# Kernel tuning notes

Measured on AMD Instinct MI355X. Metric: run time of the kernel, lower is better.

## Reference

```python
import jax, jax.numpy as jnp
import numpy as np

B, N, M, H, D = 16, 512, 16, 8, 128  # batch, nodes, neighbors, heads, input_dim
NEG_SLOPE = 0.2
EPS = 1e-5

def _glorot(key, shape):
    fan = sum(shape[-2:]) if len(shape) >= 2 else shape[-1]
    return jax.random.normal(key, shape, dtype=jnp.float32) * (2.0 / fan) ** 0.5

def setup_inputs() -> dict:
    key = jax.random.key(0)
    ks = jax.random.split(key, 12)
    h = jax.random.normal(ks[0], (B, N, D), dtype=jnp.float32)
    adj = jax.random.randint(ks[1], (B, N, M), 0, 2, dtype=jnp.int32)
    n_list = jax.random.randint(ks[2], (B, N, M), 0, N, dtype=jnp.int32)
    W = _glorot(ks[3], (H, D, D))            # per-head projection
    a_src = _glorot(ks[4], (H, D))           # attention vector, source half
    a_dst = _glorot(ks[5], (H, D))           # attention vector, neighbor half
    Wo = _glorot(ks[6], (H * D, D))          # concat-heads output projection
    ln1_g = jnp.ones((D,), jnp.float32); ln1_b = jnp.zeros((D,), jnp.float32)
    ff_w1 = _glorot(ks[7], (D, 2 * D)); ff_b1 = jnp.zeros((2 * D,), jnp.float32)
    ff_w2 = _glorot(ks[8], (2 * D, D)); ff_b2 = jnp.zeros((D,), jnp.float32)
    ln2_g = jnp.ones((D,), jnp.float32); ln2_b = jnp.zeros((D,), jnp.float32)
    return {"h": h, "adj": adj, "n_list": n_list, "W": W, "a_src": a_src,
            "a_dst": a_dst, "Wo": Wo, "ln1_g": ln1_g, "ln1_b": ln1_b,
            "ff_w1": ff_w1, "ff_b1": ff_b1, "ff_w2": ff_w2, "ff_b2": ff_b2,
            "ln2_g": ln2_g, "ln2_b": ln2_b}

def _layer_norm(x, g, b):
    mu = jnp.mean(x, axis=-1, keepdims=True)
    var = jnp.mean(jnp.square(x - mu), axis=-1, keepdims=True)
    return (x - mu) * jax.lax.rsqrt(var + EPS) * g + b

def _gat(h, adj, n_list, W, a_src, a_dst, Wo):
    Wh = jnp.einsum('bnd,hde->bnhe', h, W)                 # [B,N,H,D]
    s_src = jnp.einsum('bnhe,he->bnh', Wh, a_src)          # [B,N,H]
    s_dst = jnp.einsum('bnhe,he->bnh', Wh, a_dst)          # [B,N,H]
    gather = jax.vmap(lambda x, idx: x[idx])               # per-graph gather
    neigh = gather(Wh, n_list)                             # [B,N,M,H,D]
    s_dst_n = gather(s_dst, n_list)                        # [B,N,M,H]
    e = jax.nn.leaky_relu(s_src[:, :, None, :] + s_dst_n, NEG_SLOPE)
    e = jnp.where(adj[..., None] > 0, e, jnp.float32(-1e9))
    attn = jax.nn.softmax(e, axis=2)                       # over M neighbors
    out = jnp.einsum('bnmh,bnmhe->bnhe', attn, neigh)      # [B,N,H,D]
    return out.reshape(out.shape[0], out.shape[1], -1) @ Wo  # [B,N,D]

def reference(h, adj, n_list, W, a_src, a_dst, Wo, ln1_g, ln1_b,
              ff_w1, ff_b1, ff_w2, ff_b2, ln2_g, ln2_b):
    att = _gat(h, adj, n_list, W, a_src, a_dst, Wo)
    t = _layer_norm(att + h, ln1_g, ln1_b)
    ff = jax.nn.relu(t @ ff_w1 + ff_b1) @ ff_w2 + ff_b2
    return _layer_norm(ff + t, ln2_g, ln2_b)
```

## Files before the change

### kernel.cpp

```cpp
#include <hip/hip_runtime.h>
#include <hip/hip_bf16.h>

#define B_  16
#define N_  512
#define M_  16
#define H_  8
#define D_  128
#define BN_ 8192
#define NB  16

typedef __attribute__((ext_vector_type(4))) float          f32x4;
typedef __attribute__((ext_vector_type(4))) _Float16       f16x4;
typedef __attribute__((ext_vector_type(8))) unsigned short u16x8;
typedef __attribute__((ext_vector_type(8))) _Float16       f16x8;

static __device__ __forceinline__ float bf2f(__hip_bfloat16 x) { return __bfloat162float(x); }
static __device__ __forceinline__ unsigned short f2bu(float x) {
    __hip_bfloat16 b = __float2bfloat16(x);
    return *reinterpret_cast<unsigned short*>(&b);
}
static __device__ __forceinline__ float bu2f(unsigned short u) {
    return __uint_as_float(((unsigned int)u) << 16);
}

template <bool F32>
struct Pol {
    static __device__ __forceinline__ float ld(const void* p, int i) {
        if constexpr (F32) return ((const float*)p)[i];
        else               return bf2f(((const __hip_bfloat16*)p)[i]);
    }
    static __device__ __forceinline__ float4 ld4(const void* p, int i) {
        if constexpr (F32) return *(const float4*)((const float*)p + i);
        else {
            const ushort4 u = *(const ushort4*)((const unsigned short*)p + i);
            return make_float4(bu2f(u.x), bu2f(u.y), bu2f(u.z), bu2f(u.w));
        }
    }
    static __device__ __forceinline__ void ld8(const void* p, long i, float* v) {
        if constexpr (F32) {
            const float4 a = *(const float4*)((const float*)p + i);
            const float4 b = *(const float4*)((const float*)p + i + 4);
            v[0]=a.x; v[1]=a.y; v[2]=a.z; v[3]=a.w;
            v[4]=b.x; v[5]=b.y; v[6]=b.z; v[7]=b.w;
        } else {
            const u16x8 u = *(const u16x8*)((const unsigned short*)p + i);
            #pragma unroll
            for (int j = 0; j < 8; ++j) v[j] = bu2f(u[j]);
        }
    }
    static __device__ __forceinline__ void st8(void* p, long i, const float* v) {
        if constexpr (F32) {
            *(float4*)((float*)p + i)     = make_float4(v[0], v[1], v[2], v[3]);
            *(float4*)((float*)p + i + 4) = make_float4(v[4], v[5], v[6], v[7]);
        } else {
            u16x8 u;
            #pragma unroll
            for (int j = 0; j < 8; ++j) u[j] = f2bu(v[j]);
            *(u16x8*)((unsigned short*)p + i) = u;
        }
    }
};

static __device__ __forceinline__ bool probe_is_f32(const void* h) {
    bool is_f32 = false;
    const __hip_bfloat16* hb = (const __hip_bfloat16*)h;
    for (int i = 0; i < 128; ++i) {
        const float v = bf2f(hb[2 * i]);
        if (!(fabsf(v) < 1e4f)) is_f32 = true;
    }
    return is_f32;
}

template <bool F32>
static __device__ __forceinline__ void k0_body(
        const void* __restrict__ W,  const void* __restrict__ Wo,
        const void* __restrict__ a_src, const void* __restrict__ a_dst,
        float* __restrict__ wsrc, float* __restrict__ wdst,
        _Float16* __restrict__ WeffT, float* wrow ) {
    using P = Pol<F32>;
    const int blk = blockIdx.x;
    const int t   = threadIdx.x;
    if (blk < 512) {
        const int half = t >> 7, o = t & 127;
        const int hd = blk * 2 + half;
        wrow[half * 128 + o] = P::ld(W, hd * 128 + o);
        __syncthreads();
        const int hh = hd >> 7;
        float acc = 0.f;
        #pragma unroll 8
        for (int e = 0; e < 128; ++e)
            acc += wrow[half * 128 + e] * P::ld(Wo, (hh * 128 + e) * 128 + o);
        WeffT[(size_t)o * 1024 + hd] = (_Float16)acc;
    } else {
        const int hh = blk - 512;
        const int which = t >> 7, d = t & 127;
        const void* av = which ? a_dst : a_src;
        const int wbase = hh * (D_ * D_) + d * 128;
        float acc = 0.f;
        #pragma unroll 8
        for (int e = 0; e < 128; e += 4) {
            const float4 wv = P::ld4(W, wbase + e);
            const float4 aa = P::ld4(av, hh * 128 + e);
            acc += wv.x * aa.x + wv.y * aa.y + wv.z * aa.z + wv.w * aa.w;
        }
        (which ? wdst : wsrc)[hh * 128 + d] = acc;
    }
}

__global__ __launch_bounds__(256) void k0(
        const void* W, const void* Wo, const void* a_src, const void* a_dst,
        const void* h, float* wsrc, float* wdst, _Float16* WeffT) {
    __shared__ float wrow[2 * 128];
    if (probe_is_f32(h)) k0_body<true >(W, Wo, a_src, a_dst, wsrc, wdst, WeffT, wrow);
    else                 k0_body<false>(W, Wo, a_src, a_dst, wsrc, wdst, WeffT, wrow);
}

template <bool F32>
static __device__ __forceinline__ void k1_body(
        const void* __restrict__ h, const float* __restrict__ wsrc,
        const float* __restrict__ wdst, _Float16* __restrict__ ssrc_h,
        _Float16* __restrict__ sdst_h, float* hls , float* wls ) {
    using P = Pol<F32>;
    const int t   = threadIdx.x;
    const int bn0 = blockIdx.x * 16;
    {
        const int r = t >> 4, c0 = (t & 15) * 8;
        float v[8];
        P::ld8(h, (long)(bn0 + r) * 128 + c0, v);
        #pragma unroll
        for (int j = 0; j < 8; ++j) hls[r * 132 + c0 + j] = v[j];
        const int c = t >> 4;
        const float* wp = (c >> 3) ? wdst : wsrc;
        const int woff = (c & 7) * 128 + c0;
        #pragma unroll
        for (int j = 0; j < 8; ++j) wls[c * 132 + c0 + j] = wp[woff + j];
    }
    __syncthreads();
    const int n = t >> 4, c = t & 15;
    float acc = 0.f;
    #pragma unroll
    for (int e = 0; e < 128; e += 4) {
        const float4 hv = *(const float4*)(hls + n * 132 + e);
        const float4 wv = *(const float4*)(wls + c * 132 + e);
        acc += hv.x * wv.x + hv.y * wv.y + hv.z * wv.z + hv.w * wv.w;
    }
    const int node = bn0 + n;
    if (c < 8) ssrc_h[node * 8 + c]       = (_Float16)acc;
    else       sdst_h[node * 8 + (c - 8)] = (_Float16)acc;
}

__global__ __launch_bounds__(256) void k1(const void* h, const float* wsrc,
                                          const float* wdst, _Float16* ssrc_h,
                                          _Float16* sdst_h) {
    __shared__ float hls[16 * 132];
    __shared__ float wls[16 * 132];
    if (probe_is_f32(h)) k1_body<true >(h, wsrc, wdst, ssrc_h, sdst_h, hls, wls);
    else                 k1_body<false>(h, wsrc, wdst, ssrc_h, sdst_h, hls, wls);
}

struct __align__(16) Smem {
    union {
        _Float16 Zh[NB][1024];
        struct {
            float ts[NB][132];
            float us[NB][260];
            float ys[NB][128];
        } ff;
    } u;
    float hs[NB][128];
    union {
        float attn[NB][16][8];
        float yln[NB][128];
    } v;
    int   nls[NB][16];
    int   adjs[NB][16];
    float ssrc[NB][8];
};

template <bool F32>
static __device__ __forceinline__ void gat_body(
        Smem& s,
        const void* __restrict__ h,
        const int*  __restrict__ adj,
        const int*  __restrict__ n_list,
        const _Float16* __restrict__ ssrc_h,
        const _Float16* __restrict__ sdst_h,
        const _Float16* __restrict__ WeffT,
        const void* __restrict__ g1, const void* __restrict__ bb1,
        const void* __restrict__ w1, const void* __restrict__ fb1,
        const void* __restrict__ w2, const void* __restrict__ fb2,
        const void* __restrict__ g2, const void* __restrict__ bb2,
        void* __restrict__ out) {
    using P = Pol<F32>;
    const int t   = threadIdx.x;
    const int bn0 = blockIdx.x * NB;
    const int b   = bn0 >> 9;
    const int l   = t & 63;
    const int w   = t >> 6;
    const int lo  = l & 15;
    const int hi  = l >> 4;

    {
        const int r = t >> 4, c0 = (t & 15) * 8;
        float v[8];
        P::ld8(h, (long)(bn0 + r) * 128 + c0, v);
        #pragma unroll
        for (int j = 0; j < 8; ++j) s.hs[r][c0 + j] = v[j];
    }
    {
        const int r = t >> 4, m = t & 15;
        s.nls[r][m]  = n_list[(bn0 + r) * M_ + m] & (N_ - 1);
        s.adjs[r][m] = adj[(bn0 + r) * M_ + m];
    }
    if (t < NB * 8) s.ssrc[t >> 3][t & 7] = (float)ssrc_h[bn0 * 8 + t];
    __syncthreads();

    {
        const int r = t >> 4, m = t & 15;
        const int nbr = s.nls[r][m];
        const f16x8 sd = *(const f16x8*)(sdst_h + (size_t)(b * N_ + nbr) * 8);
        const int amask = s.adjs[r][m];
        float sc[8];
        #pragma unroll
        for (int hh = 0; hh < 8; ++hh) {
            float x = s.ssrc[r][hh] + (float)sd[hh];
            x = x > 0.f ? x : 0.2f * x;
            if (amask == 0) x = -1e9f;
            sc[hh] = x;
        }
        *(float4*)&s.v.attn[r][m][0] = make_float4(sc[0], sc[1], sc[2], sc[3]);
        *(float4*)&s.v.attn[r][m][4] = make_float4(sc[4], sc[5], sc[6], sc[7]);
    }
    __syncthreads();

    if (t < NB * 8) {
        const int r = t >> 3, hh = t & 7;
        float mx = -3.4e38f;
        #pragma unroll
        for (int m = 0; m < 16; ++m) mx = fmaxf(mx, s.v.attn[r][m][hh]);
        float ex[16], sum = 0.f;
        #pragma unroll
        for (int m = 0; m < 16; ++m) { ex[m] = __expf(s.v.attn[r][m][hh] - mx); sum += ex[m]; }
        const float inv = 1.f / sum;
        #pragma unroll
        for (int m = 0; m < 16; ++m) s.v.attn[r][m][hh] = ex[m] * inv;
    }
    __syncthreads();

    {
        const int r = t >> 4, dc = t & 15, d0 = dc * 8;
        float z[8][8];
        #pragma unroll
        for (int hh = 0; hh < 8; ++hh)
            #pragma unroll
            for (int jj = 0; jj < 8; ++jj) z[hh][jj] = 0.f;
        #pragma unroll 4
        for (int m = 0; m < 16; ++m) {
            const int nbr = s.nls[r][m];
            float hv[8];
            P::ld8(h, (long)(b * N_ + nbr) * 128 + d0, hv);
            const float4 a0 = *(const float4*)&s.v.attn[r][m][0];
            const float4 a1 = *(const float4*)&s.v.attn[r][m][4];
            const float av[8] = { a0.x, a0.y, a0.z, a0.w, a1.x, a1.y, a1.z, a1.w };
            #pragma unroll
            for (int hh = 0; hh < 8; ++hh)
                #pragma unroll
                for (int jj = 0; jj < 8; ++jj) z[hh][jj] += av[hh] * hv[jj];
        }
        char* zb = (char*)&s.u.Zh[0][0] + r * 2048;
        const int xo = (r & 7) << 4;
        #pragma unroll
        for (int hh = 0; hh < 8; ++hh) {
            f16x8 vv;
            #pragma unroll
            for (int jj = 0; jj < 8; ++jj) vv[jj] = (_Float16)z[hh][jj];
            *(f16x8*)(zb + ((hh * 256 + dc * 16) ^ xo)) = vv;
        }
    }
    __syncthreads();

    {
        const char* za  = (const char*)&s.u.Zh[0][0] + lo * 2048;
        const int   xo  = (lo & 7) << 4;
        const char* wb0 = (const char*)(WeffT + (size_t)(w * 32 + lo)      * 1024);
        const char* wb1 = (const char*)(WeffT + (size_t)(w * 32 + lo + 16) * 1024);
        f32x4 acc0 = {0.f, 0.f, 0.f, 0.f}, acc1 = {0.f, 0.f, 0.f, 0.f};
        #pragma unroll 8
        for (int ks = 0; ks < 64; ++ks) {
            const int kb = ks * 32 + hi * 8;
            const f16x4 a  = *(const f16x4*)(za + (kb ^ xo));
            const f16x4 b0 = *(const f16x4*)(wb0 + kb);
            const f16x4 b1 = *(const f16x4*)(wb1 + kb);
            acc0 = __builtin_amdgcn_mfma_f32_16x16x16f16(a, b0, acc0, 0, 0, 0);
            acc1 = __builtin_amdgcn_mfma_f32_16x16x16f16(a, b1, acc1, 0, 0, 0);
        }
        const int o0 = w * 32 + lo, o1 = o0 + 16;
        #pragma unroll
        for (int q = 0; q < 4; ++q) {
            const int rr = hi * 4 + q;
            s.v.yln[rr][o0] = acc0[q] + s.hs[rr][o0];
            s.v.yln[rr][o1] = acc1[q] + s.hs[rr][o1];
        }
    }
    __syncthreads();

    {
        const int r = t >> 4, j0 = (t & 15) * 8;
        const float4 x0 = *(const float4*)&s.v.yln[r][j0];
        const float4 x1 = *(const float4*)&s.v.yln[r][j0 + 4];
        const float x[8] = { x0.x, x0.y, x0.z, x0.w, x1.x, x1.y, x1.z, x1.w };
        float sm = 0.f, ss = 0.f;
        #pragma unroll
        for (int j = 0; j < 8; ++j) { sm += x[j]; ss += x[j] * x[j]; }
        #pragma unroll
        for (int off = 8; off > 0; off >>= 1) {
            sm += __shfl_xor(sm, off);
            ss += __shfl_xor(ss, off);
        }
        const float mu   = sm * (1.f / 128.f);
        const float var  = ss * (1.f / 128.f) - mu * mu;
        const float rstd = rsqrtf(var + 1e-5f);
        float gv[8], bv[8];
        P::ld8(g1, j0, gv);
        P::ld8(bb1, j0, bv);
        #pragma unroll
        for (int j = 0; j < 8; ++j)
            s.u.ff.ts[r][j0 + j] = (x[j] - mu) * rstd * gv[j] + bv[j];
    }
    __syncthreads();

    {
        float acc[NB];
        #pragma unroll
        for (int r = 0; r < NB; ++r) acc[r] = 0.f;
        for (int k0 = 0; k0 < 128; k0 += 4) {
            float wv[4];
            #pragma unroll
            for (int j = 0; j < 4; ++j) wv[j] = P::ld(w1, (k0 + j) * 256 + t);
            #pragma unroll
            for (int r = 0; r < NB; ++r) {
                const float4 tv = *(const float4*)&s.u.ff.ts[r][k0];
                acc[r] += tv.x * wv[0] + tv.y * wv[1] + tv.z * wv[2] + tv.w * wv[3];
            }
        }
        const float bias = P::ld(fb1, t);
        #pragma unroll
        for (int r = 0; r < NB; ++r) s.u.ff.us[r][t] = fmaxf(acc[r] + bias, 0.f);
    }
    __syncthreads();

    {
        const int e    = t & 127;
        const int half = t >> 7;
        float acc[8];
        #pragma unroll
        for (int rr = 0; rr < 8; ++rr) acc[rr] = 0.f;
        for (int k0 = 0; k0 < 256; k0 += 4) {
            float wv[4];
            #pragma unroll
            for (int j = 0; j < 4; ++j) wv[j] = P::ld(w2, (k0 + j) * 128 + e);
            #pragma unroll
            for (int rr = 0; rr < 8; ++rr) {
                const float4 uv = *(const float4*)&s.u.ff.us[half * 8 + rr][k0];
                acc[rr] += uv.x * wv[0] + uv.y * wv[1] + uv.z * wv[2] + uv.w * wv[3];
            }
        }
        const float bias = P::ld(fb2, e);
        #pragma unroll
        for (int rr = 0; rr < 8; ++rr) {
            const int r = half * 8 + rr;
            s.u.ff.ys[r][e] = acc[rr] + bias + s.u.ff.ts[r][e];
        }
    }
    __syncthreads();

    {
        const int r = t >> 4, j0 = (t & 15) * 8;
        const float4 x0 = *(const float4*)&s.u.ff.ys[r][j0];
        const float4 x1 = *(const float4*)&s.u.ff.ys[r][j0 + 4];
        const float x[8] = { x0.x, x0.y, x0.z, x0.w, x1.x, x1.y, x1.z, x1.w };
        float sm = 0.f, ss = 0.f;
        #pragma unroll
        for (int j = 0; j < 8; ++j) { sm += x[j]; ss += x[j] * x[j]; }
        #pragma unroll
        for (int off = 8; off > 0; off >>= 1) {
            sm += __shfl_xor(sm, off);
            ss += __shfl_xor(ss, off);
        }
        const float mu   = sm * (1.f / 128.f);
        const float var  = ss * (1.f / 128.f) - mu * mu;
        const float rstd = rsqrtf(var + 1e-5f);
        float gv[8], bv[8], o8[8];
        P::ld8(g2, j0, gv);
        P::ld8(bb2, j0, bv);
        #pragma unroll
        for (int j = 0; j < 8; ++j) o8[j] = (x[j] - mu) * rstd * gv[j] + bv[j];
        P::st8(out, (long)(bn0 + r) * 128 + j0, o8);
    }
}

__global__ __launch_bounds__(256) void k_gat(
        const void* __restrict__ h,
        const int*  __restrict__ adj,
        const int*  __restrict__ n_list,
        const _Float16* __restrict__ ssrc_h,
        const _Float16* __restrict__ sdst_h,
        const _Float16* __restrict__ WeffT,
        const void* __restrict__ g1, const void* __restrict__ bb1,
        const void* __restrict__ w1, const void* __restrict__ fb1,
        const void* __restrict__ w2, const void* __restrict__ fb2,
        const void* __restrict__ g2, const void* __restrict__ bb2,
        void* __restrict__ out) {
    __shared__ Smem s;
    if (probe_is_f32(h))
        gat_body<true >(s, h, adj, n_list, ssrc_h, sdst_h, WeffT,
                        g1, bb1, w1, fb1, w2, fb2, g2, bb2, out);
    else
        gat_body<false>(s, h, adj, n_list, ssrc_h, sdst_h, WeffT,
                        g1, bb1, w1, fb1, w2, fb2, g2, bb2, out);
}

extern "C" void kernel_launch(void* const* d_in, const int* in_sizes, int n_in,
                              void* d_out, int out_size, void* d_ws, size_t ws_size,
                              hipStream_t stream) {
    (void)in_sizes; (void)n_in; (void)out_size; (void)ws_size;

    char* wsb = (char*)d_ws;
    float*     wsrc  = (float*)(wsb);
    float*     wdst  = (float*)(wsb + 4096);
    _Float16*  ssrc  = (_Float16*)(wsb + 8192);
    _Float16*  sdst  = (_Float16*)(wsb + 139264);
    _Float16*  WeffT = (_Float16*)(wsb + 270336);

    k0<<<520,      256, 0, stream>>>(d_in[3], d_in[6], d_in[4], d_in[5], d_in[0],
                                     wsrc, wdst, WeffT);
    k1<<<BN_ / 16, 256, 0, stream>>>(d_in[0], wsrc, wdst, ssrc, sdst);
    k_gat<<<BN_ / NB, 256, 0, stream>>>(
        d_in[0], (const int*)d_in[1], (const int*)d_in[2], ssrc, sdst, WeffT,
        d_in[7], d_in[8], d_in[9], d_in[10], d_in[11], d_in[12],
        d_in[13], d_in[14], d_out);
}
```

Measured before the change: 174.2 us.

## Move FFN matmuls to f16 MFMA and double k_gat block size

```diff
diff --git a/kernel.cpp b/kernel.cpp
--- a/kernel.cpp
+++ b/kernel.cpp
@@ -162,9 +162,9 @@
     union {
         _Float16 Zh[NB][1024];
         struct {
-            float ts[NB][132];
-            float us[NB][260];
-            float ys[NB][128];
+            float    ts[NB][132];
+            _Float16 us[NB][260];
+            float    ys[NB][128];
         } ff;
     } u;
     float hs[NB][128];
@@ -201,13 +201,11 @@
     const int hi  = l >> 4;
 
     {
-        const int r = t >> 4, c0 = (t & 15) * 8;
-        float v[8];
-        P::ld8(h, (long)(bn0 + r) * 128 + c0, v);
-        #pragma unroll
-        for (int j = 0; j < 8; ++j) s.hs[r][c0 + j] = v[j];
-    }
-    {
+        const int r = t >> 5, c0 = (t & 31) * 4;
+        const float4 v = P::ld4(h, (bn0 + r) * 128 + c0);
+        *(float4*)&s.hs[r][c0] = v;
+    }
+    if (t < 256) {
         const int r = t >> 4, m = t & 15;
         s.nls[r][m]  = n_list[(bn0 + r) * M_ + m] & (N_ - 1);
         s.adjs[r][m] = adj[(bn0 + r) * M_ + m];
@@ -215,7 +213,7 @@
     if (t < NB * 8) s.ssrc[t >> 3][t & 7] = (float)ssrc_h[bn0 * 8 + t];
     __syncthreads();
 
-    {
+    if (t < 256) {
         const int r = t >> 4, m = t & 15;
         const int nbr = s.nls[r][m];
         const f16x8 sd = *(const f16x8*)(sdst_h + (size_t)(b * N_ + nbr) * 8);
@@ -248,33 +246,33 @@
     __syncthreads();
 
     {
-        const int r = t >> 4, dc = t & 15, d0 = dc * 8;
-        float z[8][8];
+        const int r = t >> 5, dc = t & 31, d0 = dc * 4;
+        float z[8][4];
         #pragma unroll
         for (int hh = 0; hh < 8; ++hh)
             #pragma unroll
-            for (int jj = 0; jj < 8; ++jj) z[hh][jj] = 0.f;
+            for (int jj = 0; jj < 4; ++jj) z[hh][jj] = 0.f;
         #pragma unroll 4
         for (int m = 0; m < 16; ++m) {
             const int nbr = s.nls[r][m];
-            float hv[8];
-            P::ld8(h, (long)(b * N_ + nbr) * 128 + d0, hv);
+            const float4 hv = P::ld4(h, (b * N_ + nbr) * 128 + d0);
+            const float hv4[4] = { hv.x, hv.y, hv.z, hv.w };
             const float4 a0 = *(const float4*)&s.v.attn[r][m][0];
             const float4 a1 = *(const float4*)&s.v.attn[r][m][4];
             const float av[8] = { a0.x, a0.y, a0.z, a0.w, a1.x, a1.y, a1.z, a1.w };
             #pragma unroll
             for (int hh = 0; hh < 8; ++hh)
                 #pragma unroll
-                for (int jj = 0; jj < 8; ++jj) z[hh][jj] += av[hh] * hv[jj];
+                for (int jj = 0; jj < 4; ++jj) z[hh][jj] += av[hh] * hv4[jj];
         }
         char* zb = (char*)&s.u.Zh[0][0] + r * 2048;
         const int xo = (r & 7) << 4;
         #pragma unroll
         for (int hh = 0; hh < 8; ++hh) {
-            f16x8 vv;
-            #pragma unroll
-            for (int jj = 0; jj < 8; ++jj) vv[jj] = (_Float16)z[hh][jj];
-            *(f16x8*)(zb + ((hh * 256 + dc * 16) ^ xo)) = vv;
+            f16x4 vv;
+            #pragma unroll
+            for (int jj = 0; jj < 4; ++jj) vv[jj] = (_Float16)z[hh][jj];
+            *(f16x4*)(zb + ((hh * 256 + dc * 8) ^ xo)) = vv;
         }
     }
     __syncthreads();
@@ -282,29 +280,25 @@
     {
         const char* za  = (const char*)&s.u.Zh[0][0] + lo * 2048;
         const int   xo  = (lo & 7) << 4;
-        const char* wb0 = (const char*)(WeffT + (size_t)(w * 32 + lo)      * 1024);
-        const char* wb1 = (const char*)(WeffT + (size_t)(w * 32 + lo + 16) * 1024);
-        f32x4 acc0 = {0.f, 0.f, 0.f, 0.f}, acc1 = {0.f, 0.f, 0.f, 0.f};
+        const char* wb0 = (const char*)(WeffT + (size_t)(w * 16 + lo) * 1024);
+        f32x4 acc0 = {0.f, 0.f, 0.f, 0.f};
         #pragma unroll 8
         for (int ks = 0; ks < 64; ++ks) {
             const int kb = ks * 32 + hi * 8;
             const f16x4 a  = *(const f16x4*)(za + (kb ^ xo));
             const f16x4 b0 = *(const f16x4*)(wb0 + kb);
-            const f16x4 b1 = *(const f16x4*)(wb1 + kb);
             acc0 = __builtin_amdgcn_mfma_f32_16x16x16f16(a, b0, acc0, 0, 0, 0);
-            acc1 = __builtin_amdgcn_mfma_f32_16x16x16f16(a, b1, acc1, 0, 0, 0);
-        }
-        const int o0 = w * 32 + lo, o1 = o0 + 16;
+        }
+        const int o0 = w * 16 + lo;
         #pragma unroll
         for (int q = 0; q < 4; ++q) {
             const int rr = hi * 4 + q;
             s.v.yln[rr][o0] = acc0[q] + s.hs[rr][o0];
-            s.v.yln[rr][o1] = acc1[q] + s.hs[rr][o1];
-        }
-    }
-    __syncthreads();
-
-    {
+        }
+    }
+    __syncthreads();
+
+    if (t < 256) {
         const int r = t >> 4, j0 = (t & 15) * 8;
         const float4 x0 = *(const float4*)&s.v.yln[r][j0];
         const float4 x1 = *(const float4*)&s.v.yln[r][j0 + 4];
@@ -330,51 +324,56 @@
     __syncthreads();
 
     {
-        float acc[NB];
-        #pragma unroll
-        for (int r = 0; r < NB; ++r) acc[r] = 0.f;
-        for (int k0 = 0; k0 < 128; k0 += 4) {
-            float wv[4];
-            #pragma unroll
-            for (int j = 0; j < 4; ++j) wv[j] = P::ld(w1, (k0 + j) * 256 + t);
-            #pragma unroll
-            for (int r = 0; r < NB; ++r) {
-                const float4 tv = *(const float4*)&s.u.ff.ts[r][k0];
-                acc[r] += tv.x * wv[0] + tv.y * wv[1] + tv.z * wv[2] + tv.w * wv[3];
+        f32x4 acc[2] = { {0.f,0.f,0.f,0.f}, {0.f,0.f,0.f,0.f} };
+        #pragma unroll
+        for (int ks = 0; ks < 8; ++ks) {
+            const int k = ks * 16 + hi * 4;
+            const float4 tv = *(const float4*)&s.u.ff.ts[lo][k];
+            f16x4 a;
+            a[0] = (_Float16)tv.x; a[1] = (_Float16)tv.y;
+            a[2] = (_Float16)tv.z; a[3] = (_Float16)tv.w;
+            #pragma unroll
+            for (int nt = 0; nt < 2; ++nt) {
+                const int o = w * 32 + nt * 16 + lo;
+                f16x4 bb;
+                #pragma unroll
+                for (int j = 0; j < 4; ++j) bb[j] = (_Float16)P::ld(w1, (k + j) * 256 + o);
+                acc[nt] = __builtin_amdgcn_mfma_f32_16x16x16f16(a, bb, acc[nt], 0, 0, 0);
             }
         }
-        const float bias = P::ld(fb1, t);
-        #pragma unroll
-        for (int r = 0; r < NB; ++r) s.u.ff.us[r][t] = fmaxf(acc[r] + bias, 0.f);
-    }
-    __syncthreads();
-
-    {
-        const int e    = t & 127;
-        const int half = t >> 7;
-        float acc[8];
-        #pragma unroll
-        for (int rr = 0; rr < 8; ++rr) acc[rr] = 0.f;
-        for (int k0 = 0; k0 < 256; k0 += 4) {
-            float wv[4];
-            #pragma unroll
-            for (int j = 0; j < 4; ++j) wv[j] = P::ld(w2, (k0 + j) * 128 + e);
-            #pragma unroll
-            for (int rr = 0; rr < 8; ++rr) {
-                const float4 uv = *(const float4*)&s.u.ff.us[half * 8 + rr][k0];
-                acc[rr] += uv.x * wv[0] + uv.y * wv[1] + uv.z * wv[2] + uv.w * wv[3];
-            }
-        }
-        const float bias = P::ld(fb2, e);
-        #pragma unroll
-        for (int rr = 0; rr < 8; ++rr) {
-            const int r = half * 8 + rr;
-            s.u.ff.ys[r][e] = acc[rr] + bias + s.u.ff.ts[r][e];
-        }
-    }
-    __syncthreads();
-
-    {
+        #pragma unroll
+        for (int nt = 0; nt < 2; ++nt) {
+            const int o = w * 32 + nt * 16 + lo;
+            const float bias = P::ld(fb1, o);
+            #pragma unroll
+            for (int q = 0; q < 4; ++q)
+                s.u.ff.us[hi * 4 + q][o] = (_Float16)fmaxf(acc[nt][q] + bias, 0.f);
+        }
+    }
+    __syncthreads();
+
+    {
+        const int o0 = w * 16 + lo;
+        f32x4 acc = {0.f, 0.f, 0.f, 0.f};
+        #pragma unroll
+        for (int ks = 0; ks < 16; ++ks) {
+            const int k = ks * 16 + hi * 4;
+            const f16x4 a = *(const f16x4*)&s.u.ff.us[lo][k];
+            f16x4 bb;
+            #pragma unroll
+            for (int j = 0; j < 4; ++j) bb[j] = (_Float16)P::ld(w2, (k + j) * 128 + o0);
+            acc = __builtin_amdgcn_mfma_f32_16x16x16f16(a, bb, acc, 0, 0, 0);
+        }
+        const float bias = P::ld(fb2, o0);
+        #pragma unroll
+        for (int q = 0; q < 4; ++q) {
+            const int rr = hi * 4 + q;
+            s.u.ff.ys[rr][o0] = acc[q] + bias + s.u.ff.ts[rr][o0];
+        }
+    }
+    __syncthreads();
+
+    if (t < 256) {
         const int r = t >> 4, j0 = (t & 15) * 8;
         const float4 x0 = *(const float4*)&s.u.ff.ys[r][j0];
         const float4 x1 = *(const float4*)&s.u.ff.ys[r][j0 + 4];
@@ -399,7 +398,7 @@
     }
 }
 
-__global__ __launch_bounds__(256) void k_gat(
+__global__ __launch_bounds__(512) void k_gat(
         const void* __restrict__ h,
         const int*  __restrict__ adj,
         const int*  __restrict__ n_list,
@@ -435,7 +434,7 @@
     k0<<<520,      256, 0, stream>>>(d_in[3], d_in[6], d_in[4], d_in[5], d_in[0],
                                      wsrc, wdst, WeffT);
     k1<<<BN_ / 16, 256, 0, stream>>>(d_in[0], wsrc, wdst, ssrc, sdst);
-    k_gat<<<BN_ / NB, 256, 0, stream>>>(
+    k_gat<<<BN_ / NB, 512, 0, stream>>>(
         d_in[0], (const int*)d_in[1], (const int*)d_in[2], ssrc, sdst, WeffT,
         d_in[7], d_in[8], d_in[9], d_in[10], d_in[11], d_in[12],
         d_in[13], d_in[14], d_out);
```

Measured after the change: 158.9 us. 1.1x faster.
